# Optimization experiments

Measured on AMD Instinct MI355X. Metric: run time of the kernel, lower is better.

Reference implementation:

```python
import jax, jax.numpy as jnp
import numpy as np

N = 10000      # nodes
E = 160000     # edges (before self-loops)
IN = 128       # input channels
H1, C1 = 8, 128   # layer-1 heads / per-head channels
OUT = 64       # output channels
NEG_SLOPE = 0.2   # PyG GATConv leaky_relu slope


def _glorot(key, shape):
    fan = shape[0] + shape[-1]
    return jax.random.normal(key, shape, jnp.float32) * np.float32(np.sqrt(2.0 / fan))


def setup_inputs() -> dict:
    key = jax.random.key(0)
    ks = jax.random.split(key, 10)
    x = jax.random.normal(ks[0], (N, IN), jnp.float32)
    edge_index = jax.random.randint(ks[1], (2, E), 0, N, dtype=jnp.int64)
    return {
        "x": x,
        "edge_index": edge_index,
        "W1": _glorot(ks[2], (IN, H1 * C1)),
        "a_src1": _glorot(ks[3], (H1, C1)),
        "a_dst1": _glorot(ks[4], (H1, C1)),
        "b1": jnp.zeros((H1 * C1,), jnp.float32),
        "W2": _glorot(ks[5], (H1 * C1, OUT)),
        "a_src2": _glorot(ks[6], (1, OUT)),
        "a_dst2": _glorot(ks[7], (1, OUT)),
        "b2": jnp.zeros((OUT,), jnp.float32),
    }


def gat_conv(x, src, dst, W, a_src, a_dst, bias, heads, ch, concat):
    n = x.shape[0]
    h = (x @ W).reshape(n, heads, ch)                 # [N,H,C]
    alpha_s = jnp.sum(h * a_src, axis=-1)             # [N,H]
    alpha_d = jnp.sum(h * a_dst, axis=-1)             # [N,H]
    e = jax.nn.leaky_relu(alpha_s[src] + alpha_d[dst], NEG_SLOPE)  # [E',H]
    # segment softmax over incoming edges of each dst node
    m = jax.ops.segment_max(e, dst, num_segments=n)
    e = jnp.exp(e - m[dst])
    s = jax.ops.segment_sum(e, dst, num_segments=n)
    alpha = e / (s[dst] + 1e-16)                      # [E',H]
    msg = h[src] * alpha[:, :, None]                  # [E',H,C]
    out = jax.ops.segment_sum(msg, dst, num_segments=n)  # [N,H,C]
    out = out.reshape(n, heads * ch) if concat else jnp.mean(out, axis=1)
    return out + bias


def reference(x, edge_index, W1, a_src1, a_dst1, b1, W2, a_src2, a_dst2, b2):
    n = x.shape[0]
    loops = jnp.arange(n, dtype=edge_index.dtype)     # PyG add_self_loops=True
    src = jnp.concatenate([edge_index[0], loops])
    dst = jnp.concatenate([edge_index[1], loops])
    h = jax.nn.elu(gat_conv(x, src, dst, W1, a_src1, a_dst1, b1, H1, C1, True))
    # dropout is identity in eval mode
    return gat_conv(h, src, dst, W2, a_src2, a_dst2, b2, 1, OUT, False)
```

## Files before the change

kernel.cpp:

```cpp
#include <hip/hip_runtime.h>
#include <math.h>


#define NEG_SLOPE 0.2f

typedef short bf16x8 __attribute__((ext_vector_type(8)));
typedef float f32x4 __attribute__((ext_vector_type(4)));

__device__ __forceinline__ float leaky(float v) { return v >= 0.0f ? v : NEG_SLOPE * v; }

__device__ __forceinline__ unsigned short f2bf(float f) {
    unsigned u = __float_as_uint(f);
    u += 0x7FFFu + ((u >> 16) & 1u);
    return (unsigned short)(u >> 16);
}


__global__ __launch_bounds__(256) void init_k(
    const float* __restrict__ W1, const float* __restrict__ a_src1,
    const float* __restrict__ a_dst1, const float* __restrict__ W2,
    float* __restrict__ As_t, float* __restrict__ Ad_t,
    unsigned short* __restrict__ W1bT, unsigned short* __restrict__ W2bT,
    int* __restrict__ counts, int N) {
    int b = blockIdx.x;
    int nzb = (N + 255) >> 8;
    if (b < nzb) {
        int i = b * 256 + threadIdx.x;
        if (i < N) counts[i] = 0;
        return;
    }
    b -= nzb;
    if (b < 4) {
        int i = b * 256 + threadIdx.x;
        int k = i >> 3, h = i & 7;
        float ss = 0.f, sd = 0.f;
        for (int c = 0; c < 128; c += 4) {
            float4 w = *(const float4*)(W1 + (size_t)k * 1024 + h * 128 + c);
            float4 a = *(const float4*)(a_src1 + h * 128 + c);
            float4 d = *(const float4*)(a_dst1 + h * 128 + c);
            ss += w.x * a.x + w.y * a.y + w.z * a.z + w.w * a.w;
            sd += w.x * d.x + w.y * d.y + w.z * d.z + w.w * d.w;
        }
        As_t[h * 132 + k] = ss;
        Ad_t[h * 132 + k] = sd;
        return;
    }
    b -= 4;
    __shared__ unsigned short tile[32][33];
    if (b < 128) {
        int kt = b & 3, hct = b >> 2;
        int j = threadIdx.x & 31;
        int i0 = threadIdx.x >> 5;
        for (int i = i0; i < 32; i += 8)
            tile[i][j] = f2bf(W1[(size_t)(kt * 32 + i) * 1024 + hct * 32 + j]);
        __syncthreads();
        for (int i = i0; i < 32; i += 8) {
            int hc = hct * 32 + i, k = kt * 32 + j;
            int h = hc >> 7, c = hc & 127;
            W1bT[h * 16384 + c * 128 + k] = tile[j][i];
        }
    } else {
        b -= 128;
        int kt = b & 31, ctile = b >> 5;
        int j = threadIdx.x & 31;
        int i0 = threadIdx.x >> 5;
        for (int i = i0; i < 32; i += 8)
            tile[i][j] = f2bf(W2[(size_t)(kt * 32 + i) * 64 + ctile * 32 + j]);
        __syncthreads();
        for (int i = i0; i < 32; i += 8)
            W2bT[(size_t)(ctile * 32 + i) * 1024 + kt * 32 + j] = tile[j][i];
    }
}


__global__ __launch_bounds__(1024) void alpha_fill(
    const float* __restrict__ x, const float* __restrict__ As_t, const float* __restrict__ Ad_t,
    const int* __restrict__ ei, int* __restrict__ counts,
    float* __restrict__ as1, float* __restrict__ ad1,
    int* __restrict__ srcs, int E, int N, int nb_alpha) {
    int t = threadIdx.x;
    if ((int)blockIdx.x < nb_alpha) {
        __shared__ float sAs[1056], sAd[1056];
        for (int i = t; i < 1056; i += 1024) {
            sAs[i] = As_t[i];
            sAd[i] = Ad_t[i];
        }
        __syncthreads();
        int node = blockIdx.x * 128 + (t >> 3);
        int h = t & 7;
        if (node >= N) return;
        const float* sa = sAs + h * 132;
        const float* sd = sAd + h * 132;
        float accs = 0.f, accd = 0.f;
        for (int k = 0; k < 128; k += 4) {
            float4 xv = *(const float4*)(x + (size_t)node * 128 + k);
            float4 av = *(const float4*)(sa + k);
            float4 dv = *(const float4*)(sd + k);
            accs += xv.x * av.x + xv.y * av.y + xv.z * av.z + xv.w * av.w;
            accd += xv.x * dv.x + xv.y * dv.y + xv.z * dv.z + xv.w * dv.w;
        }
        as1[node * 8 + h] = accs;
        ad1[node * 8 + h] = accd;
    } else {
        int i = ((int)blockIdx.x - nb_alpha) * 1024 + t;
        int M = E + N;
        if (i >= M) return;
        int src, dst;
        if (i < E) { src = ei[i]; dst = ei[E + i]; }
        else       { src = dst = i - E; }
        int slot = atomicAdd(&counts[dst], 1);
        if (slot < 64) srcs[dst * 64 + slot] = src;
    }
}


__global__ __launch_bounds__(256) void l1_gather(
    const float* __restrict__ x, const float* __restrict__ as1,
    const float* __restrict__ ad1, const int* __restrict__ counts,
    const int* __restrict__ srcs, unsigned short* __restrict__ y_b, int N) {
    int wid = threadIdx.x >> 6;
    int n = blockIdx.x * 4 + wid;
    if (n >= N) return;
    int lane = threadIdx.x & 63;
    int beg = n * 64;
    int deg = counts[n];
    deg = deg < 64 ? deg : 64;
    __shared__ float wls[4][64][8];
    int sv = srcs[beg + (lane < deg ? lane : 0)];
    {
        float4 a0 = *(const float4*)(as1 + (size_t)sv * 8);
        float4 a1 = *(const float4*)(as1 + (size_t)sv * 8 + 4);
        float4 b0 = *(const float4*)(ad1 + (size_t)n * 8);
        float4 b1 = *(const float4*)(ad1 + (size_t)n * 8 + 4);
        if (lane < deg) {
            float4 w0, w1;
            w0.x = __expf(leaky(a0.x + b0.x));
            w0.y = __expf(leaky(a0.y + b0.y));
            w0.z = __expf(leaky(a0.z + b0.z));
            w0.w = __expf(leaky(a0.w + b0.w));
            w1.x = __expf(leaky(a1.x + b1.x));
            w1.y = __expf(leaky(a1.y + b1.y));
            w1.z = __expf(leaky(a1.z + b1.z));
            w1.w = __expf(leaky(a1.w + b1.w));
            *(float4*)&wls[wid][lane][0] = w0;
            *(float4*)&wls[wid][lane][4] = w1;
        }
    }
    float2 acc[8];
#pragma unroll
    for (int h = 0; h < 8; h++) acc[h] = make_float2(0.f, 0.f);
    float4 ws0 = make_float4(0.f, 0.f, 0.f, 0.f);
    float4 ws1 = make_float4(0.f, 0.f, 0.f, 0.f);
    const float* xb = x + lane * 2;
#define L1G_BODY(E_, SRC)                                                        \
    {                                                                            \
        float4 w0_ = *(const float4*)&wls[wid][E_][0];                           \
        float4 w1_ = *(const float4*)&wls[wid][E_][4];                           \
        float2 xv_ = *(const float2*)(xb + (size_t)(SRC) * 128);                 \
        ws0.x += w0_.x; ws0.y += w0_.y; ws0.z += w0_.z; ws0.w += w0_.w;          \
        ws1.x += w1_.x; ws1.y += w1_.y; ws1.z += w1_.z; ws1.w += w1_.w;          \
        acc[0].x = fmaf(w0_.x, xv_.x, acc[0].x); acc[0].y = fmaf(w0_.x, xv_.y, acc[0].y); \
        acc[1].x = fmaf(w0_.y, xv_.x, acc[1].x); acc[1].y = fmaf(w0_.y, xv_.y, acc[1].y); \
        acc[2].x = fmaf(w0_.z, xv_.x, acc[2].x); acc[2].y = fmaf(w0_.z, xv_.y, acc[2].y); \
        acc[3].x = fmaf(w0_.w, xv_.x, acc[3].x); acc[3].y = fmaf(w0_.w, xv_.y, acc[3].y); \
        acc[4].x = fmaf(w1_.x, xv_.x, acc[4].x); acc[4].y = fmaf(w1_.x, xv_.y, acc[4].y); \
        acc[5].x = fmaf(w1_.y, xv_.x, acc[5].x); acc[5].y = fmaf(w1_.y, xv_.y, acc[5].y); \
        acc[6].x = fmaf(w1_.z, xv_.x, acc[6].x); acc[6].y = fmaf(w1_.z, xv_.y, acc[6].y); \
        acc[7].x = fmaf(w1_.w, xv_.x, acc[7].x); acc[7].y = fmaf(w1_.w, xv_.y, acc[7].y); \
    }
    int i = 0;
    for (; i + 4 <= deg; i += 4) {
        int s0 = __shfl(sv, i);
        int s1 = __shfl(sv, i + 1);
        int s2 = __shfl(sv, i + 2);
        int s3 = __shfl(sv, i + 3);
        L1G_BODY(i, s0)
        L1G_BODY(i + 1, s1)
        L1G_BODY(i + 2, s2)
        L1G_BODY(i + 3, s3)
    }
    for (; i < deg; i++) {
        int s = __shfl(sv, i);
        L1G_BODY(i, s)
    }
#undef L1G_BODY
    float inv[8] = {1.f / (ws0.x + 1e-16f), 1.f / (ws0.y + 1e-16f),
                    1.f / (ws0.z + 1e-16f), 1.f / (ws0.w + 1e-16f),
                    1.f / (ws1.x + 1e-16f), 1.f / (ws1.y + 1e-16f),
                    1.f / (ws1.z + 1e-16f), 1.f / (ws1.w + 1e-16f)};
    unsigned short* dst = y_b + (size_t)n * 1024 + lane * 2;
#pragma unroll
    for (int h = 0; h < 8; h++) {
        unsigned lo = f2bf(acc[h].x * inv[h]);
        unsigned hi = f2bf(acc[h].y * inv[h]);
        *(unsigned*)(dst + h * 128) = lo | (hi << 16);
    }
}


__global__ __launch_bounds__(256) void l12_gemm(
    const unsigned short* __restrict__ y_b, const unsigned short* __restrict__ W1bT,
    const float* __restrict__ b1, const unsigned short* __restrict__ W2bT,
    const float* __restrict__ a_src2, const float* __restrict__ a_dst2,
    float* __restrict__ h2, float* __restrict__ as2, float* __restrict__ ad2, int N) {
    int nb = blockIdx.x * 16;
    int w = threadIdx.x >> 6;
    int lane = threadIdx.x & 63;
    int n16 = lane & 15, quad = lane >> 4;
    __shared__ unsigned short hb[16 * 1032];
    __shared__ float sA[4][16], sD[4][16];
    int node_a = nb + n16;
    const unsigned short* yrow = y_b + (size_t)(node_a < N ? node_a : 0) * 1024;
#pragma unroll
    for (int cti = 0; cti < 16; cti++) {
        int ct = w * 16 + cti;
        int h = ct >> 3;
        int cc = (ct & 7) * 16;
        const unsigned short* Wh = W1bT + h * 16384 + (size_t)(cc + n16) * 128 + quad * 8;
        const unsigned short* ya = yrow + h * 128 + quad * 8;
        f32x4 acc = (f32x4){0.f, 0.f, 0.f, 0.f};
#pragma unroll
        for (int ks = 0; ks < 4; ks++) {
            bf16x8 a = *(const bf16x8*)(ya + ks * 32);
            bf16x8 b = *(const bf16x8*)(Wh + ks * 32);
            acc = __builtin_amdgcn_mfma_f32_16x16x32_bf16(a, b, acc, 0, 0, 0);
        }
        int c = h * 128 + cc + n16;
        float bias = b1[c];
#pragma unroll
        for (int r = 0; r < 4; r++) {
            float v = acc[r] + bias;
            v = v > 0.f ? v : expm1f(v);
            hb[(quad * 4 + r) * 1032 + c] = f2bf(v);
        }
    }
    __syncthreads();
    const unsigned short* arow = hb + n16 * 1032 + quad * 8;
    const unsigned short* brow = W2bT + (size_t)(w * 16 + n16) * 1024 + quad * 8;
    f32x4 acc = (f32x4){0.f, 0.f, 0.f, 0.f};
#pragma unroll 8
    for (int ks = 0; ks < 32; ks++) {
        bf16x8 a = *(const bf16x8*)(arow + ks * 32);
        bf16x8 b = *(const bf16x8*)(brow + ks * 32);
        acc = __builtin_amdgcn_mfma_f32_16x16x32_bf16(a, b, acc, 0, 0, 0);
    }
    int c2 = w * 16 + n16;
    float asc = a_src2[c2], adc = a_dst2[c2];
    float pav[4], pdv[4];
#pragma unroll
    for (int r = 0; r < 4; r++) {
        int node = nb + quad * 4 + r;
        if (node < N) h2[(size_t)node * 64 + c2] = acc[r];
        pav[r] = acc[r] * asc;
        pdv[r] = acc[r] * adc;
#pragma unroll
        for (int mm = 1; mm <= 8; mm <<= 1) {
            pav[r] += __shfl_xor(pav[r], mm);
            pdv[r] += __shfl_xor(pdv[r], mm);
        }
    }
    if (n16 == 0) {
#pragma unroll
        for (int r = 0; r < 4; r++) {
            sA[w][quad * 4 + r] = pav[r];
            sD[w][quad * 4 + r] = pdv[r];
        }
    }
    __syncthreads();
    if (threadIdx.x < 16) {
        int node = nb + threadIdx.x;
        if (node < N) {
            as2[node] = sA[0][threadIdx.x] + sA[1][threadIdx.x] + sA[2][threadIdx.x] + sA[3][threadIdx.x];
            ad2[node] = sD[0][threadIdx.x] + sD[1][threadIdx.x] + sD[2][threadIdx.x] + sD[3][threadIdx.x];
        }
    }
}


__global__ __launch_bounds__(256) void l2_gather(
    const float* __restrict__ h2, const float* __restrict__ as2,
    const float* __restrict__ ad2, const float* __restrict__ b2,
    const int* __restrict__ counts, const int* __restrict__ srcs,
    float* __restrict__ out, int N) {
    int n = blockIdx.x * 4 + (threadIdx.x >> 6);
    if (n >= N) return;
    int lane = threadIdx.x & 63;
    int beg = n * 64;
    int deg = counts[n];
    deg = deg < 64 ? deg : 64;
    float adn = ad2[n];
    float acc = 0.f;
    int sv = srcs[beg + (lane < deg ? lane : 0)];
    float wv = (lane < deg) ? __expf(leaky(as2[sv] + adn)) : 0.f;
    int i = 0;
    for (; i + 4 <= deg; i += 4) {
        int s0 = __shfl(sv, i),     s1 = __shfl(sv, i + 1);
        int s2 = __shfl(sv, i + 2), s3 = __shfl(sv, i + 3);
        float w0 = __shfl(wv, i),     w1 = __shfl(wv, i + 1);
        float w2 = __shfl(wv, i + 2), w3 = __shfl(wv, i + 3);
        float v0 = h2[(size_t)s0 * 64 + lane];
        float v1 = h2[(size_t)s1 * 64 + lane];
        float v2 = h2[(size_t)s2 * 64 + lane];
        float v3 = h2[(size_t)s3 * 64 + lane];
        acc = fmaf(w0, v0, acc);
        acc = fmaf(w1, v1, acc);
        acc = fmaf(w2, v2, acc);
        acc = fmaf(w3, v3, acc);
    }
    for (; i < deg; i++) {
        int s = __shfl(sv, i);
        float ww = __shfl(wv, i);
        acc = fmaf(ww, h2[(size_t)s * 64 + lane], acc);
    }
    float wsum = wv;
#pragma unroll
    for (int mm = 1; mm <= 32; mm <<= 1) wsum += __shfl_xor(wsum, mm);
    out[(size_t)n * 64 + lane] = acc / (wsum + 1e-16f) + b2[lane];
}


static inline size_t align_up(size_t v, size_t a) { return (v + a - 1) / a * a; }

extern "C" void kernel_launch(void* const* d_in, const int* in_sizes, int n_in,
                              void* d_out, int out_size, void* d_ws, size_t ws_size,
                              hipStream_t stream) {
    const float* x      = (const float*)d_in[0];
    const int*   ei     = (const int*)d_in[1];
    const float* W1     = (const float*)d_in[2];
    const float* a_src1 = (const float*)d_in[3];
    const float* a_dst1 = (const float*)d_in[4];
    const float* b1     = (const float*)d_in[5];
    const float* W2     = (const float*)d_in[6];
    const float* a_src2 = (const float*)d_in[7];
    const float* a_dst2 = (const float*)d_in[8];
    const float* b2     = (const float*)d_in[9];
    float* out = (float*)d_out;

    int N = in_sizes[0] / 128;
    int E = in_sizes[1] / 2;
    int M = E + N;

    char* p = (char*)d_ws;
    size_t off = 0;
    auto carve = [&](size_t bytes) {
        void* r = p + off;
        off = align_up(off + bytes, 256);
        return r;
    };
    int*            counts  = (int*)carve((size_t)N * 4);
    int*            srcs    = (int*)carve((size_t)N * 64 * 4);
    float*          As_t    = (float*)carve(1056 * 4);
    float*          Ad_t    = (float*)carve(1056 * 4);
    float*          as1     = (float*)carve((size_t)N * 8 * 4);
    float*          ad1     = (float*)carve((size_t)N * 8 * 4);
    float*          as2     = (float*)carve((size_t)N * 4);
    float*          ad2     = (float*)carve((size_t)N * 4);
    float*          h2      = (float*)carve((size_t)N * 64 * 4);
    unsigned short* W1bT    = (unsigned short*)carve((size_t)8 * 128 * 128 * 2);
    unsigned short* W2bT    = (unsigned short*)carve((size_t)64 * 1024 * 2);
    unsigned short* y_b     = (unsigned short*)carve((size_t)N * 1024 * 2);
    (void)ws_size;

    int nzb      = (N + 255) / 256;
    int nb_alpha = (N + 127) / 128;
    int nb_fill  = (M + 1023) / 1024;

    init_k<<<nzb + 4 + 192, 256, 0, stream>>>(W1, a_src1, a_dst1, W2,
                                              As_t, Ad_t, W1bT, W2bT, counts, N);
    alpha_fill<<<nb_alpha + nb_fill, 1024, 0, stream>>>(x, As_t, Ad_t, ei, counts,
                                                        as1, ad1, srcs, E, N, nb_alpha);
    l1_gather<<<(N + 3) / 4, 256, 0, stream>>>(x, as1, ad1, counts, srcs, y_b, N);
    l12_gemm<<<(N + 15) / 16, 256, 0, stream>>>(y_b, W1bT, b1, W2bT, a_src2, a_dst2,
                                                h2, as2, ad2, N);
    l2_gather<<<(N + 3) / 4, 256, 0, stream>>>(h2, as2, ad2, b2, counts, srcs, out, N);
}
```

Measured before the change: 162.2 us.

## Fuse all GAT stages into one persistent cooperative kernel with grid syncs

Replaces the five separate kernel launches with a single cooperative persistent kernel that runs each stage as a grid-stride loop and separates the stages with grid.sync(). It is meant to remove per-launch overhead and the idle gaps between launches. In exchange, the grid is capped at resident blocks, so each block runs many work items per stage, and grid-wide barriers add their own cost. The old multi-kernel path stays as a fallback when cooperative launch is unavailable.

```diff
diff --git a/kernel.cpp b/kernel.cpp
--- a/kernel.cpp
+++ b/kernel.cpp
@@ -1,5 +1,8 @@
 #include <hip/hip_runtime.h>
+#include <hip/hip_cooperative_groups.h>
 #include <math.h>
+
+namespace cg = cooperative_groups;
 
 
 #define NEG_SLOPE 0.2f
@@ -13,6 +16,301 @@
     unsigned u = __float_as_uint(f);
     u += 0x7FFFu + ((u >> 16) & 1u);
     return (unsigned short)(u >> 16);
+}
+
+
+__global__ __launch_bounds__(256, 4) void mega(
+    const float* __restrict__ x, const int* __restrict__ ei,
+    const float* __restrict__ W1, const float* __restrict__ a_src1,
+    const float* __restrict__ a_dst1, const float* __restrict__ b1,
+    const float* __restrict__ W2, const float* __restrict__ a_src2,
+    const float* __restrict__ a_dst2, const float* __restrict__ b2,
+    float* __restrict__ out,
+    int* __restrict__ counts, int* __restrict__ srcs,
+    float* __restrict__ As_t, float* __restrict__ Ad_t,
+    float* __restrict__ as1, float* __restrict__ ad1,
+    float* __restrict__ as2, float* __restrict__ ad2,
+    float* __restrict__ h2,
+    unsigned short* __restrict__ W1bT, unsigned short* __restrict__ W2bT,
+    unsigned short* __restrict__ y_b,
+    int E, int N) {
+    cg::grid_group grid = cg::this_grid();
+    const int nb = (int)gridDim.x, bid = (int)blockIdx.x, t = (int)threadIdx.x;
+    const int gtid = bid * 256 + t, gsize = nb * 256;
+    const int M = E + N;
+    __shared__ __align__(16) char smraw[33664];
+
+    for (int i = gtid; i < N; i += gsize) counts[i] = 0;
+    for (int i = gtid; i < 1024; i += gsize) {
+        int k = i >> 3, h = i & 7;
+        float ss = 0.f, sd = 0.f;
+        for (int c = 0; c < 128; c += 4) {
+            float4 w = *(const float4*)(W1 + (size_t)k * 1024 + h * 128 + c);
+            float4 a = *(const float4*)(a_src1 + h * 128 + c);
+            float4 d = *(const float4*)(a_dst1 + h * 128 + c);
+            ss += w.x * a.x + w.y * a.y + w.z * a.z + w.w * a.w;
+            sd += w.x * d.x + w.y * d.y + w.z * d.z + w.w * d.w;
+        }
+        As_t[h * 132 + k] = ss;
+        Ad_t[h * 132 + k] = sd;
+    }
+    {
+        typedef unsigned short row33[33];
+        row33* tile = (row33*)smraw;
+        int j = t & 31, i0 = t >> 5;
+        for (int job = bid; job < 192; job += nb) {
+            __syncthreads();
+            if (job < 128) {
+                int kt = job & 3, hct = job >> 2;
+                for (int i = i0; i < 32; i += 8)
+                    tile[i][j] = f2bf(W1[(size_t)(kt * 32 + i) * 1024 + hct * 32 + j]);
+                __syncthreads();
+                for (int i = i0; i < 32; i += 8) {
+                    int hc = hct * 32 + i, k = kt * 32 + j;
+                    int h = hc >> 7, c = hc & 127;
+                    W1bT[h * 16384 + c * 128 + k] = tile[j][i];
+                }
+            } else {
+                int jb = job - 128;
+                int kt = jb & 31, ctile = jb >> 5;
+                for (int i = i0; i < 32; i += 8)
+                    tile[i][j] = f2bf(W2[(size_t)(kt * 32 + i) * 64 + ctile * 32 + j]);
+                __syncthreads();
+                for (int i = i0; i < 32; i += 8)
+                    W2bT[(size_t)(ctile * 32 + i) * 1024 + kt * 32 + j] = tile[j][i];
+            }
+        }
+    }
+    grid.sync();
+
+    {
+        float* sAs = (float*)smraw;
+        float* sAd = sAs + 1056;
+        for (int i = t; i < 1056; i += 256) { sAs[i] = As_t[i]; sAd[i] = Ad_t[i]; }
+        __syncthreads();
+        int h = t & 7, tn = t >> 3;
+        const float* sa = sAs + h * 132;
+        const float* sd = sAd + h * 132;
+        for (int base = bid * 32; base < N; base += nb * 32) {
+            int node = base + tn;
+            if (node < N) {
+                float accs = 0.f, accd = 0.f;
+                for (int k = 0; k < 128; k += 4) {
+                    float4 xv = *(const float4*)(x + (size_t)node * 128 + k);
+                    float4 av = *(const float4*)(sa + k);
+                    float4 dv = *(const float4*)(sd + k);
+                    accs += xv.x * av.x + xv.y * av.y + xv.z * av.z + xv.w * av.w;
+                    accd += xv.x * dv.x + xv.y * dv.y + xv.z * dv.z + xv.w * dv.w;
+                }
+                as1[node * 8 + h] = accs;
+                ad1[node * 8 + h] = accd;
+            }
+        }
+        for (int i = gtid; i < M; i += gsize) {
+            int src, dst;
+            if (i < E) { src = ei[i]; dst = ei[E + i]; }
+            else       { src = dst = i - E; }
+            int slot = atomicAdd(&counts[dst], 1);
+            if (slot < 64) srcs[dst * 64 + slot] = src;
+        }
+    }
+    grid.sync();
+
+    {
+        int wid = t >> 6, lane = t & 63;
+        float* wl = (float*)smraw + (size_t)wid * 64 * 8;
+        const float* xb = x + lane * 2;
+        for (int n = bid * 4 + wid; n < N; n += nb * 4) {
+            int beg = n * 64;
+            int deg = counts[n];
+            deg = deg < 64 ? deg : 64;
+            int sv = srcs[beg + (lane < deg ? lane : 0)];
+            {
+                float4 ga0 = *(const float4*)(as1 + (size_t)sv * 8);
+                float4 ga1 = *(const float4*)(as1 + (size_t)sv * 8 + 4);
+                float4 gb0 = *(const float4*)(ad1 + (size_t)n * 8);
+                float4 gb1 = *(const float4*)(ad1 + (size_t)n * 8 + 4);
+                if (lane < deg) {
+                    float4 w0, w1;
+                    w0.x = __expf(leaky(ga0.x + gb0.x));
+                    w0.y = __expf(leaky(ga0.y + gb0.y));
+                    w0.z = __expf(leaky(ga0.z + gb0.z));
+                    w0.w = __expf(leaky(ga0.w + gb0.w));
+                    w1.x = __expf(leaky(ga1.x + gb1.x));
+                    w1.y = __expf(leaky(ga1.y + gb1.y));
+                    w1.z = __expf(leaky(ga1.z + gb1.z));
+                    w1.w = __expf(leaky(ga1.w + gb1.w));
+                    *(float4*)(wl + lane * 8)     = w0;
+                    *(float4*)(wl + lane * 8 + 4) = w1;
+                }
+            }
+            float2 acc[8];
+#pragma unroll
+            for (int h = 0; h < 8; h++) acc[h] = make_float2(0.f, 0.f);
+            float4 ws0 = make_float4(0.f, 0.f, 0.f, 0.f);
+            float4 ws1 = make_float4(0.f, 0.f, 0.f, 0.f);
+#define L1G_BODY(E_, SRC)                                                        \
+    {                                                                            \
+        float4 w0_ = *(const float4*)(wl + (E_) * 8);                            \
+        float4 w1_ = *(const float4*)(wl + (E_) * 8 + 4);                        \
+        float2 xv_ = *(const float2*)(xb + (size_t)(SRC) * 128);                 \
+        ws0.x += w0_.x; ws0.y += w0_.y; ws0.z += w0_.z; ws0.w += w0_.w;          \
+        ws1.x += w1_.x; ws1.y += w1_.y; ws1.z += w1_.z; ws1.w += w1_.w;          \
+        acc[0].x = fmaf(w0_.x, xv_.x, acc[0].x); acc[0].y = fmaf(w0_.x, xv_.y, acc[0].y); \
+        acc[1].x = fmaf(w0_.y, xv_.x, acc[1].x); acc[1].y = fmaf(w0_.y, xv_.y, acc[1].y); \
+        acc[2].x = fmaf(w0_.z, xv_.x, acc[2].x); acc[2].y = fmaf(w0_.z, xv_.y, acc[2].y); \
+        acc[3].x = fmaf(w0_.w, xv_.x, acc[3].x); acc[3].y = fmaf(w0_.w, xv_.y, acc[3].y); \
+        acc[4].x = fmaf(w1_.x, xv_.x, acc[4].x); acc[4].y = fmaf(w1_.x, xv_.y, acc[4].y); \
+        acc[5].x = fmaf(w1_.y, xv_.x, acc[5].x); acc[5].y = fmaf(w1_.y, xv_.y, acc[5].y); \
+        acc[6].x = fmaf(w1_.z, xv_.x, acc[6].x); acc[6].y = fmaf(w1_.z, xv_.y, acc[6].y); \
+        acc[7].x = fmaf(w1_.w, xv_.x, acc[7].x); acc[7].y = fmaf(w1_.w, xv_.y, acc[7].y); \
+    }
+            int i = 0;
+            for (; i + 4 <= deg; i += 4) {
+                int s0 = __shfl(sv, i);
+                int s1 = __shfl(sv, i + 1);
+                int s2 = __shfl(sv, i + 2);
+                int s3 = __shfl(sv, i + 3);
+                L1G_BODY(i, s0)
+                L1G_BODY(i + 1, s1)
+                L1G_BODY(i + 2, s2)
+                L1G_BODY(i + 3, s3)
+            }
+            for (; i < deg; i++) {
+                int s = __shfl(sv, i);
+                L1G_BODY(i, s)
+            }
+#undef L1G_BODY
+            float inv[8] = {1.f / (ws0.x + 1e-16f), 1.f / (ws0.y + 1e-16f),
+                            1.f / (ws0.z + 1e-16f), 1.f / (ws0.w + 1e-16f),
+                            1.f / (ws1.x + 1e-16f), 1.f / (ws1.y + 1e-16f),
+                            1.f / (ws1.z + 1e-16f), 1.f / (ws1.w + 1e-16f)};
+            unsigned short* dst = y_b + (size_t)n * 1024 + lane * 2;
+#pragma unroll
+            for (int h = 0; h < 8; h++) {
+                unsigned lo = f2bf(acc[h].x * inv[h]);
+                unsigned hi = f2bf(acc[h].y * inv[h]);
+                *(unsigned*)(dst + h * 128) = lo | (hi << 16);
+            }
+        }
+    }
+    grid.sync();
+
+    {
+        unsigned short* hb = (unsigned short*)smraw;
+        float* sAp = (float*)(smraw + 33024);
+        float* sDp = (float*)(smraw + 33024 + 256);
+        int w = t >> 6, lane = t & 63;
+        int n16 = lane & 15, quad = lane >> 4;
+        int ntiles = (N + 15) >> 4;
+        for (int tl = bid; tl < ntiles; tl += nb) {
+            __syncthreads();
+            int nbase = tl * 16;
+            int node_a = nbase + n16;
+            const unsigned short* yrow = y_b + (size_t)(node_a < N ? node_a : 0) * 1024;
+#pragma unroll
+            for (int cti = 0; cti < 16; cti++) {
+                int ct = w * 16 + cti;
+                int h = ct >> 3;
+                int cc = (ct & 7) * 16;
+                const unsigned short* Wh = W1bT + h * 16384 + (size_t)(cc + n16) * 128 + quad * 8;
+                const unsigned short* ya = yrow + h * 128 + quad * 8;
+                f32x4 acc = (f32x4){0.f, 0.f, 0.f, 0.f};
+#pragma unroll
+                for (int ks = 0; ks < 4; ks++) {
+                    bf16x8 a = *(const bf16x8*)(ya + ks * 32);
+                    bf16x8 b = *(const bf16x8*)(Wh + ks * 32);
+                    acc = __builtin_amdgcn_mfma_f32_16x16x32_bf16(a, b, acc, 0, 0, 0);
+                }
+                int c = h * 128 + cc + n16;
+                float bias = b1[c];
+#pragma unroll
+                for (int r = 0; r < 4; r++) {
+                    float v = acc[r] + bias;
+                    v = v > 0.f ? v : expm1f(v);
+                    hb[(quad * 4 + r) * 1032 + c] = f2bf(v);
+                }
+            }
+            __syncthreads();
+            const unsigned short* arow = hb + n16 * 1032 + quad * 8;
+            const unsigned short* brow = W2bT + (size_t)(w * 16 + n16) * 1024 + quad * 8;
+            f32x4 acc = (f32x4){0.f, 0.f, 0.f, 0.f};
+#pragma unroll 8
+            for (int ks = 0; ks < 32; ks++) {
+                bf16x8 a = *(const bf16x8*)(arow + ks * 32);
+                bf16x8 b = *(const bf16x8*)(brow + ks * 32);
+                acc = __builtin_amdgcn_mfma_f32_16x16x32_bf16(a, b, acc, 0, 0, 0);
+            }
+            int c2 = w * 16 + n16;
+            float asc = a_src2[c2], adc = a_dst2[c2];
+            float pav[4], pdv[4];
+#pragma unroll
+            for (int r = 0; r < 4; r++) {
+                int node = nbase + quad * 4 + r;
+                if (node < N) h2[(size_t)node * 64 + c2] = acc[r];
+                pav[r] = acc[r] * asc;
+                pdv[r] = acc[r] * adc;
+#pragma unroll
+                for (int mm = 1; mm <= 8; mm <<= 1) {
+                    pav[r] += __shfl_xor(pav[r], mm);
+                    pdv[r] += __shfl_xor(pdv[r], mm);
+                }
+            }
+            if (n16 == 0) {
+#pragma unroll
+                for (int r = 0; r < 4; r++) {
+                    sAp[w * 16 + quad * 4 + r] = pav[r];
+                    sDp[w * 16 + quad * 4 + r] = pdv[r];
+                }
+            }
+            __syncthreads();
+            if (t < 16) {
+                int node = nbase + t;
+                if (node < N) {
+                    as2[node] = sAp[t] + sAp[16 + t] + sAp[32 + t] + sAp[48 + t];
+                    ad2[node] = sDp[t] + sDp[16 + t] + sDp[32 + t] + sDp[48 + t];
+                }
+            }
+        }
+    }
+    grid.sync();
+
+    {
+        int wid = t >> 6, lane = t & 63;
+        for (int n = bid * 4 + wid; n < N; n += nb * 4) {
+            int beg = n * 64;
+            int deg = counts[n];
+            deg = deg < 64 ? deg : 64;
+            float adn = ad2[n];
+            float accv = 0.f;
+            int sv = srcs[beg + (lane < deg ? lane : 0)];
+            float wv = (lane < deg) ? __expf(leaky(as2[sv] + adn)) : 0.f;
+            int i = 0;
+            for (; i + 4 <= deg; i += 4) {
+                int s0 = __shfl(sv, i),     s1 = __shfl(sv, i + 1);
+                int s2 = __shfl(sv, i + 2), s3 = __shfl(sv, i + 3);
+                float w0 = __shfl(wv, i),     w1 = __shfl(wv, i + 1);
+                float w2 = __shfl(wv, i + 2), w3 = __shfl(wv, i + 3);
+                float v0 = h2[(size_t)s0 * 64 + lane];
+                float v1 = h2[(size_t)s1 * 64 + lane];
+                float v2 = h2[(size_t)s2 * 64 + lane];
+                float v3 = h2[(size_t)s3 * 64 + lane];
+                accv = fmaf(w0, v0, accv);
+                accv = fmaf(w1, v1, accv);
+                accv = fmaf(w2, v2, accv);
+                accv = fmaf(w3, v3, accv);
+            }
+            for (; i < deg; i++) {
+                int s = __shfl(sv, i);
+                float ww = __shfl(wv, i);
+                accv = fmaf(ww, h2[(size_t)s * 64 + lane], accv);
+            }
+            float wsum = wv;
+#pragma unroll
+            for (int mm = 1; mm <= 32; mm <<= 1) wsum += __shfl_xor(wsum, mm);
+            out[(size_t)n * 64 + lane] = accv / (wsum + 1e-16f) + b2[lane];
+        }
+    }
 }
 
 
@@ -72,7 +370,6 @@
     }
 }
 
-
 __global__ __launch_bounds__(1024) void alpha_fill(
     const float* __restrict__ x, const float* __restrict__ As_t, const float* __restrict__ Ad_t,
     const int* __restrict__ ei, int* __restrict__ counts,
@@ -112,7 +409,6 @@
         if (slot < 64) srcs[dst * 64 + slot] = src;
     }
 }
-
 
 __global__ __launch_bounds__(256) void l1_gather(
     const float* __restrict__ x, const float* __restrict__ as1,
@@ -197,7 +493,6 @@
     }
 }
 
-
 __global__ __launch_bounds__(256) void l12_gemm(
     const unsigned short* __restrict__ y_b, const unsigned short* __restrict__ W1bT,
     const float* __restrict__ b1, const unsigned short* __restrict__ W2bT,
@@ -275,7 +570,6 @@
         }
     }
 }
-
 
 __global__ __launch_bounds__(256) void l2_gather(
     const float* __restrict__ h2, const float* __restrict__ as2,
@@ -361,16 +655,46 @@
     unsigned short* y_b     = (unsigned short*)carve((size_t)N * 1024 * 2);
     (void)ws_size;
 
-    int nzb      = (N + 255) / 256;
-    int nb_alpha = (N + 127) / 128;
-    int nb_fill  = (M + 1023) / 1024;
-
-    init_k<<<nzb + 4 + 192, 256, 0, stream>>>(W1, a_src1, a_dst1, W2,
-                                              As_t, Ad_t, W1bT, W2bT, counts, N);
-    alpha_fill<<<nb_alpha + nb_fill, 1024, 0, stream>>>(x, As_t, Ad_t, ei, counts,
-                                                        as1, ad1, srcs, E, N, nb_alpha);
-    l1_gather<<<(N + 3) / 4, 256, 0, stream>>>(x, as1, ad1, counts, srcs, y_b, N);
-    l12_gemm<<<(N + 15) / 16, 256, 0, stream>>>(y_b, W1bT, b1, W2bT, a_src2, a_dst2,
-                                                h2, as2, ad2, N);
-    l2_gather<<<(N + 3) / 4, 256, 0, stream>>>(h2, as2, ad2, b2, counts, srcs, out, N);
+    static int s_grid = -2;
+    if (s_grid == -2) {
+        int coop = 0, ncu = 0, bpc = 0;
+        hipError_t e1 = hipDeviceGetAttribute(&coop, hipDeviceAttributeCooperativeLaunch, 0);
+        hipError_t e2 = hipDeviceGetAttribute(&ncu, hipDeviceAttributeMultiprocessorCount, 0);
+        hipError_t e3 = hipOccupancyMaxActiveBlocksPerMultiprocessor(&bpc, mega, 256, 0);
+        if (e1 == hipSuccess && e2 == hipSuccess && e3 == hipSuccess &&
+            coop && bpc >= 1 && ncu >= 1) {
+            long g = (long)bpc * (long)ncu;
+            if (g > 2048) g = 2048;
+            s_grid = (int)g;
+        } else {
+            s_grid = -1;
+        }
+    }
+
+    bool done = false;
+    if (s_grid > 0) {
+        void* kargs[] = {
+            (void*)&x, (void*)&ei, (void*)&W1, (void*)&a_src1, (void*)&a_dst1,
+            (void*)&b1, (void*)&W2, (void*)&a_src2, (void*)&a_dst2, (void*)&b2,
+            (void*)&out, (void*)&counts, (void*)&srcs, (void*)&As_t, (void*)&Ad_t,
+            (void*)&as1, (void*)&ad1, (void*)&as2, (void*)&ad2, (void*)&h2,
+            (void*)&W1bT, (void*)&W2bT, (void*)&y_b, (void*)&E, (void*)&N};
+        hipError_t le = hipLaunchCooperativeKernel((const void*)mega, dim3(s_grid),
+                                                   dim3(256), kargs, 0, stream);
+        done = (le == hipSuccess);
+        if (!done) s_grid = -1;
+    }
+    if (!done) {
+        int nzb      = (N + 255) / 256;
+        int nb_alpha = (N + 127) / 128;
+        int nb_fill  = (M + 1023) / 1024;
+        init_k<<<nzb + 4 + 192, 256, 0, stream>>>(W1, a_src1, a_dst1, W2,
+                                                  As_t, Ad_t, W1bT, W2bT, counts, N);
+        alpha_fill<<<nb_alpha + nb_fill, 1024, 0, stream>>>(x, As_t, Ad_t, ei, counts,
+                                                            as1, ad1, srcs, E, N, nb_alpha);
+        l1_gather<<<(N + 3) / 4, 256, 0, stream>>>(x, as1, ad1, counts, srcs, y_b, N);
+        l12_gemm<<<(N + 15) / 16, 256, 0, stream>>>(y_b, W1bT, b1, W2bT, a_src2, a_dst2,
+                                                    h2, as2, ad2, N);
+        l2_gather<<<(N + 3) / 4, 256, 0, stream>>>(h2, as2, ad2, b2, counts, srcs, out, N);
+    }
 }
```

Measured after the change: 423.0 us. 161% more time.
